# Kernel optimization log

Hardware: AMD Instinct MI355X
Metric: run time of the kernel (lower is better)

Reference implementation:

```python
import jax, jax.numpy as jnp
import numpy as np

NEG_SLOPE = 0.2
BN_EPS = 1e-5
SM_EPS = 1e-16


def gatv2_conv(x, src, dst, num_nodes, Wl, bl, Wr, br, att, bias, concat):
    # x: [N, Fin]; att: [H, C]
    H, C = att.shape
    xl = (x @ Wl + bl).reshape(-1, H, C)  # source-side (x_j), lin_l
    xr = (x @ Wr + br).reshape(-1, H, C)  # target-side (x_i), lin_r
    e = jax.nn.leaky_relu(xl[src] + xr[dst], NEG_SLOPE)          # [E, H, C]
    logits = jnp.einsum('ehc,hc->eh', e, att)                    # [E, H]
    m = jax.ops.segment_max(logits, dst, num_segments=num_nodes)  # [N, H]
    expv = jnp.exp(logits - m[dst])
    denom = jax.ops.segment_sum(expv, dst, num_segments=num_nodes)
    alpha = expv / (denom[dst] + SM_EPS)                          # [E, H]
    msg = xl[src] * alpha[:, :, None]                             # [E, H, C]
    out = jax.ops.segment_sum(msg, dst, num_segments=num_nodes)   # [N, H, C]
    out = out.reshape(num_nodes, H * C) if concat else out.mean(axis=1)
    return out + bias


def batchnorm(x, gamma, beta):
    mean = x.mean(axis=0)
    var = x.var(axis=0)  # biased, as torch uses for normalization
    return gamma * (x - mean) * jax.lax.rsqrt(var + BN_EPS) + beta


def setup_inputs() -> dict:
    key = jax.random.key(0)
    ks = jax.random.split(key, 16)
    N, E = 50000, 800000
    Fin, Hid, Out, H = 128, 64, 64, 4
    s = 0.05
    inp = {
        'x': jax.random.normal(ks[0], (N, Fin), jnp.float32),
        'edge_index': jax.random.randint(ks[1], (2, E), 0, N, jnp.int64),
        # conv1 (heads=4, concat=False)
        'Wl1': jax.random.normal(ks[2], (Fin, H * Hid), jnp.float32) * s,
        'bl1': jnp.zeros((H * Hid,), jnp.float32),
        'Wr1': jax.random.normal(ks[3], (Fin, H * Hid), jnp.float32) * s,
        'br1': jnp.zeros((H * Hid,), jnp.float32),
        'att1': jax.random.normal(ks[4], (H, Hid), jnp.float32) * s,
        'bias1': jnp.zeros((Hid,), jnp.float32),
        'g1': jnp.ones((Hid,), jnp.float32),
        'beta1': jnp.zeros((Hid,), jnp.float32),
        # conv2 (heads=1, concat=True -> same as single head)
        'Wl2': jax.random.normal(ks[5], (Hid, Out), jnp.float32) * s,
        'bl2': jnp.zeros((Out,), jnp.float32),
        'Wr2': jax.random.normal(ks[6], (Hid, Out), jnp.float32) * s,
        'br2': jnp.zeros((Out,), jnp.float32),
        'att2': jax.random.normal(ks[7], (1, Out), jnp.float32) * s,
        'bias2': jnp.zeros((Out,), jnp.float32),
        'g2': jnp.ones((Out,), jnp.float32),
        'beta2': jnp.zeros((Out,), jnp.float32),
    }
    return inp


def reference(x, edge_index, Wl1, bl1, Wr1, br1, att1, bias1, g1, beta1,
              Wl2, bl2, Wr2, br2, att2, bias2, g2, beta2):
    N = x.shape[0]
    loops = jnp.arange(N, dtype=edge_index.dtype)  # PyG add_self_loops=True
    src = jnp.concatenate([edge_index[0], loops])
    dst = jnp.concatenate([edge_index[1], loops])
    h = gatv2_conv(x, src, dst, N, Wl1, bl1, Wr1, br1, att1, bias1, concat=False)
    h = jax.nn.relu(batchnorm(h, g1, beta1))  # dropout = identity (eval)
    h = gatv2_conv(h, src, dst, N, Wl2, bl2, Wr2, br2, att2, bias2, concat=True)
    h = jax.nn.relu(batchnorm(h, g2, beta2))
    return h
```

## Files before the change

### kernel.cpp

```cpp
#include <hip/hip_runtime.h>
#include <hip/hip_bf16.h>
#include <math.h>

#define TPB 256

typedef __attribute__((ext_vector_type(8))) short bfrag8;
typedef __attribute__((ext_vector_type(4))) float f32x4;

static __device__ __forceinline__ float bf2f(unsigned int u) {
  union { unsigned int i; float f; } c; c.i = u << 16; return c.f;
}
static __device__ __forceinline__ unsigned short f2bf(float f) {
  union { float f; unsigned int i; } c; c.f = f;
  unsigned int lsb = (c.i >> 16) & 1u;
  return (unsigned short)((c.i + 0x7fffu + lsb) >> 16);
}
static __device__ __forceinline__ float lrelu(float v) {
  return v > 0.f ? v : 0.2f * v;
}

__global__ void k_deg(const int* __restrict__ ei, int E, int ET, int* __restrict__ deg) {
  int e = blockIdx.x * blockDim.x + threadIdx.x;
  if (e >= ET) return;
  int dst = (e < E) ? ei[E + e] : (e - E);
  atomicAdd(&deg[dst], 1);
}

__global__ void k_scan1(const int* __restrict__ deg, int N, int* __restrict__ bsum) {
  __shared__ int sm[TPB];
  int i = blockIdx.x * TPB + threadIdx.x;
  sm[threadIdx.x] = (i < N) ? deg[i] : 0;
  __syncthreads();
  for (int d = TPB / 2; d > 0; d >>= 1) {
    if (threadIdx.x < d) sm[threadIdx.x] += sm[threadIdx.x + d];
    __syncthreads();
  }
  if (threadIdx.x == 0) bsum[blockIdx.x] = sm[0];
}

__global__ void k_scan2(const int* __restrict__ bsum, int SB, int* __restrict__ bpre,
                        int* __restrict__ rowoff, int N) {
  __shared__ int sm[TPB];
  int v = (threadIdx.x < SB) ? bsum[threadIdx.x] : 0;
  sm[threadIdx.x] = v;
  __syncthreads();
  for (int d = 1; d < TPB; d <<= 1) {
    int t = (threadIdx.x >= d) ? sm[threadIdx.x - d] : 0;
    __syncthreads();
    sm[threadIdx.x] += t;
    __syncthreads();
  }
  if (threadIdx.x < SB) bpre[threadIdx.x] = sm[threadIdx.x] - v;
  if (threadIdx.x == SB - 1) rowoff[N] = sm[SB - 1];
}

__global__ void k_scan3(const int* __restrict__ deg, const int* __restrict__ bpre,
                        int N, int* __restrict__ rowoff, int* __restrict__ cursor) {
  __shared__ int sm[TPB];
  int i = blockIdx.x * TPB + threadIdx.x;
  int v = (i < N) ? deg[i] : 0;
  sm[threadIdx.x] = v;
  __syncthreads();
  for (int d = 1; d < TPB; d <<= 1) {
    int t = (threadIdx.x >= d) ? sm[threadIdx.x - d] : 0;
    __syncthreads();
    sm[threadIdx.x] += t;
    __syncthreads();
  }
  if (i < N) {
    int off = bpre[blockIdx.x] + sm[threadIdx.x] - v;
    rowoff[i] = off;
    cursor[i] = off;
  }
}

__global__ void k_fill(const int* __restrict__ ei, int E, int ET,
                       int* __restrict__ cursor, int* __restrict__ csrc) {
  int e = blockIdx.x * blockDim.x + threadIdx.x;
  if (e >= ET) return;
  int src, dst;
  if (e < E) { src = ei[e]; dst = ei[E + e]; } else { src = dst = e - E; }
  int pos = atomicAdd(&cursor[dst], 1);
  csrc[pos] = src;
}

__global__ void k_gemm_mfma(const float* __restrict__ A,
                            const float* __restrict__ W0, const float* __restrict__ b0,
                            const float* __restrict__ W1, const float* __restrict__ b1,
                            unsigned short* __restrict__ out0, unsigned short* __restrict__ out1,
                            int M, int K, int Nc, const float* __restrict__ affine) {
  __shared__ short As[64 * 128];
  __shared__ short Bls[64 * 128];
  __shared__ short Brs[64 * 128];
  const int r0 = blockIdx.x * 64, n0 = blockIdx.y * 64;
  const int tid = threadIdx.x;
  const int Kb = K * 2;

  const int kq = K >> 2;
  for (int idx = tid; idx < 16 * K; idx += TPB) {
    int row = idx / kq, c4 = idx - row * kq;
    int gr = r0 + row;
    float4 v = make_float4(0.f, 0.f, 0.f, 0.f);
    if (gr < M) v = *(const float4*)(A + (size_t)gr * K + c4 * 4);
    if (affine) {
      int c = c4 * 4;
      v.x = fmaxf(v.x * affine[c + 0] + affine[64 + c + 0], 0.f);
      v.y = fmaxf(v.y * affine[c + 1] + affine[64 + c + 1], 0.f);
      v.z = fmaxf(v.z * affine[c + 2] + affine[64 + c + 2], 0.f);
      v.w = fmaxf(v.w * affine[c + 3] + affine[64 + c + 3], 0.f);
    }
    ushort4 pk; pk.x = f2bf(v.x); pk.y = f2bf(v.y); pk.z = f2bf(v.z); pk.w = f2bf(v.w);
    int kb = (c4 * 8) ^ ((row & 7) << 4);
    *(ushort4*)((char*)As + row * Kb + kb) = pk;
  }
  for (int idx = tid; idx < 16 * K; idx += TPB) {
    int c = idx & 63, k4 = (idx >> 6) << 2;
    const float* p0 = W0 + (size_t)k4 * Nc + n0 + c;
    const float* p1 = W1 + (size_t)k4 * Nc + n0 + c;
    ushort4 pk0, pk1;
    pk0.x = f2bf(p0[0]); pk0.y = f2bf(p0[Nc]); pk0.z = f2bf(p0[2 * Nc]); pk0.w = f2bf(p0[3 * Nc]);
    pk1.x = f2bf(p1[0]); pk1.y = f2bf(p1[Nc]); pk1.z = f2bf(p1[2 * Nc]); pk1.w = f2bf(p1[3 * Nc]);
    int kb = (k4 * 2) ^ ((c & 7) << 4);
    *(ushort4*)((char*)Bls + c * Kb + kb) = pk0;
    *(ushort4*)((char*)Brs + c * Kb + kb) = pk1;
  }
  __syncthreads();

  const int w = tid >> 6, lane = tid & 63;
  const int arow = w * 16 + (lane & 15);
  const int l16 = (lane >> 4) << 3;
  f32x4 accL[4], accR[4];
#pragma unroll
  for (int i = 0; i < 4; ++i) { accL[i] = (f32x4)0.f; accR[i] = (f32x4)0.f; }
  for (int k0 = 0; k0 < K; k0 += 32) {
    int kb = (k0 + l16) * 2;
    bfrag8 af = *(bfrag8*)((char*)As + arow * Kb + (kb ^ ((arow & 7) << 4)));
#pragma unroll
    for (int cf = 0; cf < 4; ++cf) {
      int col = cf * 16 + (lane & 15);
      int cb = col * Kb + (kb ^ ((col & 7) << 4));
      bfrag8 bl = *(bfrag8*)((char*)Bls + cb);
      accL[cf] = __builtin_amdgcn_mfma_f32_16x16x32_bf16(af, bl, accL[cf], 0, 0, 0);
      bfrag8 br = *(bfrag8*)((char*)Brs + cb);
      accR[cf] = __builtin_amdgcn_mfma_f32_16x16x32_bf16(af, br, accR[cf], 0, 0, 0);
    }
  }
  const int rbase = r0 + w * 16 + ((lane >> 4) << 2);
  const int cbase = n0 + (lane & 15);
#pragma unroll
  for (int cf = 0; cf < 4; ++cf) {
    int gcol = cbase + cf * 16;
    float bb0 = b0[gcol], bb1 = b1[gcol];
#pragma unroll
    for (int r = 0; r < 4; ++r) {
      int grow = rbase + r;
      if (grow < M) {
        out0[(size_t)grow * Nc + gcol] = f2bf(accL[cf][r] + bb0);
        out1[(size_t)grow * Nc + gcol] = f2bf(accR[cf][r] + bb1);
      }
    }
  }
}

__global__ void k_gat1(const unsigned short* __restrict__ xl,
                       const unsigned short* __restrict__ xr,
                       const int* __restrict__ rowoff, const int* __restrict__ csrc,
                       const float* __restrict__ att, const float* __restrict__ bias,
                       float* __restrict__ out, int N) {
  int node = (blockIdx.x * blockDim.x + threadIdx.x) >> 6;
  int lane = threadIdx.x & 63;
  if (node >= N) return;
  int l4 = lane * 4;
  uint2 rv = *(const uint2*)(xr + (size_t)node * 256 + l4);
  float xr0 = bf2f(rv.x & 0xffffu), xr1 = bf2f(rv.x >> 16);
  float xr2 = bf2f(rv.y & 0xffffu), xr3 = bf2f(rv.y >> 16);
  float4 at = *(const float4*)(att + l4);
  int beg = rowoff[node], end = rowoff[node + 1];
  float s = 0.f, a0 = 0.f, a1 = 0.f, a2 = 0.f, a3 = 0.f;
  int k = beg;
  for (; k + 4 <= end; k += 4) {
    int srcs[4];
#pragma unroll
    for (int u = 0; u < 4; ++u) srcs[u] = csrc[k + u];
    uint2 vv[4];
#pragma unroll
    for (int u = 0; u < 4; ++u) vv[u] = *(const uint2*)(xl + (size_t)srcs[u] * 256 + l4);
    float xs[4][4], ps[4];
#pragma unroll
    for (int u = 0; u < 4; ++u) {
      xs[u][0] = bf2f(vv[u].x & 0xffffu); xs[u][1] = bf2f(vv[u].x >> 16);
      xs[u][2] = bf2f(vv[u].y & 0xffffu); xs[u][3] = bf2f(vv[u].y >> 16);
      ps[u] = lrelu(xs[u][0] + xr0) * at.x + lrelu(xs[u][1] + xr1) * at.y
            + lrelu(xs[u][2] + xr2) * at.z + lrelu(xs[u][3] + xr3) * at.w;
    }
#pragma unroll
    for (int u = 0; u < 4; ++u) {
      ps[u] += __shfl_xor(ps[u], 1); ps[u] += __shfl_xor(ps[u], 2);
      ps[u] += __shfl_xor(ps[u], 4); ps[u] += __shfl_xor(ps[u], 8);
    }
#pragma unroll
    for (int u = 0; u < 4; ++u) {
      float w = __expf(ps[u]);
      s += w;
      a0 += w * xs[u][0]; a1 += w * xs[u][1];
      a2 += w * xs[u][2]; a3 += w * xs[u][3];
    }
  }
  for (; k < end; ++k) {
    int src = csrc[k];
    uint2 v = *(const uint2*)(xl + (size_t)src * 256 + l4);
    float x0 = bf2f(v.x & 0xffffu), x1 = bf2f(v.x >> 16);
    float x2 = bf2f(v.y & 0xffffu), x3 = bf2f(v.y >> 16);
    float p = lrelu(x0 + xr0) * at.x + lrelu(x1 + xr1) * at.y
            + lrelu(x2 + xr2) * at.z + lrelu(x3 + xr3) * at.w;
    p += __shfl_xor(p, 1); p += __shfl_xor(p, 2);
    p += __shfl_xor(p, 4); p += __shfl_xor(p, 8);
    float w = __expf(p);
    s += w;
    a0 += w * x0; a1 += w * x1; a2 += w * x2; a3 += w * x3;
  }
  float inv = 1.f / (s + 1e-16f);
  a0 *= inv; a1 *= inv; a2 *= inv; a3 *= inv;
  a0 += __shfl_xor(a0, 16); a0 += __shfl_xor(a0, 32);
  a1 += __shfl_xor(a1, 16); a1 += __shfl_xor(a1, 32);
  a2 += __shfl_xor(a2, 16); a2 += __shfl_xor(a2, 32);
  a3 += __shfl_xor(a3, 16); a3 += __shfl_xor(a3, 32);
  if (lane < 16) {
    float4 o;
    o.x = a0 * 0.25f + bias[l4 + 0];
    o.y = a1 * 0.25f + bias[l4 + 1];
    o.z = a2 * 0.25f + bias[l4 + 2];
    o.w = a3 * 0.25f + bias[l4 + 3];
    *(float4*)(out + (size_t)node * 64 + l4) = o;
  }
}

__global__ void k_gat2(const unsigned short* __restrict__ xl,
                       const unsigned short* __restrict__ xr,
                       const int* __restrict__ rowoff, const int* __restrict__ csrc,
                       const float* __restrict__ att, const float* __restrict__ bias,
                       float* __restrict__ out, int N) {
  int node = (blockIdx.x * blockDim.x + threadIdx.x) >> 6;
  int lane = threadIdx.x & 63;
  if (node >= N) return;
  int grp = lane >> 4, c4 = (lane & 15) * 4;
  uint2 rv = *(const uint2*)(xr + (size_t)node * 64 + c4);
  float xr0 = bf2f(rv.x & 0xffffu), xr1 = bf2f(rv.x >> 16);
  float xr2 = bf2f(rv.y & 0xffffu), xr3 = bf2f(rv.y >> 16);
  float4 at = *(const float4*)(att + c4);
  int beg = rowoff[node], end = rowoff[node + 1];
  int iters = (end - beg + 3) >> 2;
  float s = 0.f, a0 = 0.f, a1 = 0.f, a2 = 0.f, a3 = 0.f;
  for (int it = 0; it < iters; ++it) {
    int kk = beg + it * 4 + grp;
    bool ok = kk < end;
    int src = ok ? csrc[kk] : 0;
    uint2 v = *(const uint2*)(xl + (size_t)src * 64 + c4);
    float x0 = bf2f(v.x & 0xffffu), x1 = bf2f(v.x >> 16);
    float x2 = bf2f(v.y & 0xffffu), x3 = bf2f(v.y >> 16);
    float p = lrelu(x0 + xr0) * at.x + lrelu(x1 + xr1) * at.y
            + lrelu(x2 + xr2) * at.z + lrelu(x3 + xr3) * at.w;
    p += __shfl_xor(p, 1); p += __shfl_xor(p, 2);
    p += __shfl_xor(p, 4); p += __shfl_xor(p, 8);
    float w = ok ? __expf(p) : 0.f;
    s += w;
    a0 += w * x0; a1 += w * x1; a2 += w * x2; a3 += w * x3;
  }
  s  += __shfl_xor(s, 16);  s  += __shfl_xor(s, 32);
  a0 += __shfl_xor(a0, 16); a0 += __shfl_xor(a0, 32);
  a1 += __shfl_xor(a1, 16); a1 += __shfl_xor(a1, 32);
  a2 += __shfl_xor(a2, 16); a2 += __shfl_xor(a2, 32);
  a3 += __shfl_xor(a3, 16); a3 += __shfl_xor(a3, 32);
  if (lane < 16) {
    float inv = 1.f / (s + 1e-16f);
    float4 o;
    o.x = a0 * inv + bias[c4 + 0];
    o.y = a1 * inv + bias[c4 + 1];
    o.z = a2 * inv + bias[c4 + 2];
    o.w = a3 * inv + bias[c4 + 3];
    *(float4*)(out + (size_t)node * 64 + c4) = o;
  }
}

__global__ void k_bnstat(const float* __restrict__ in, int N, float* __restrict__ part) {
  __shared__ float sm[TPB], sq[TPB];
  int col = threadIdx.x & 63;
  int rq = threadIdx.x >> 6;
  float s = 0.f, q = 0.f;
  for (int r = blockIdx.x * 4 + rq; r < N; r += gridDim.x * 4) {
    float v = in[(size_t)r * 64 + col];
    s += v; q += v * v;
  }
  sm[threadIdx.x] = s; sq[threadIdx.x] = q;
  __syncthreads();
  if (threadIdx.x < 64) {
    s = sm[threadIdx.x] + sm[threadIdx.x + 64] + sm[threadIdx.x + 128] + sm[threadIdx.x + 192];
    q = sq[threadIdx.x] + sq[threadIdx.x + 64] + sq[threadIdx.x + 128] + sq[threadIdx.x + 192];
    part[(size_t)blockIdx.x * 128 + threadIdx.x] = s;
    part[(size_t)blockIdx.x * 128 + 64 + threadIdx.x] = q;
  }
}

__global__ void k_bnfin(const float* __restrict__ part, int B, int N,
                        const float* __restrict__ g, const float* __restrict__ beta,
                        float* __restrict__ ab) {
  int c = threadIdx.x;
  float s = 0.f, q = 0.f;
  for (int b = 0; b < B; ++b) {
    s += part[(size_t)b * 128 + c];
    q += part[(size_t)b * 128 + 64 + c];
  }
  float mean = s / (float)N;
  float var = q / (float)N - mean * mean;
  float a = g[c] * rsqrtf(var + 1e-5f);
  ab[c] = a;
  ab[64 + c] = beta[c] - mean * a;
}

__global__ void k_bnapply(const float* __restrict__ in, const float* __restrict__ ab,
                          float* __restrict__ out, int total4) {
  int idx = blockIdx.x * blockDim.x + threadIdx.x;
  if (idx >= total4) return;
  float4 v = *(const float4*)(in + (size_t)idx * 4);
  int c0 = (idx & 15) * 4;
  v.x = fmaxf(v.x * ab[c0 + 0] + ab[64 + c0 + 0], 0.f);
  v.y = fmaxf(v.y * ab[c0 + 1] + ab[64 + c0 + 1], 0.f);
  v.z = fmaxf(v.z * ab[c0 + 2] + ab[64 + c0 + 2], 0.f);
  v.w = fmaxf(v.w * ab[c0 + 3] + ab[64 + c0 + 3], 0.f);
  *(float4*)(out + (size_t)idx * 4) = v;
}

extern "C" void kernel_launch(void* const* d_in, const int* in_sizes, int n_in,
                              void* d_out, int out_size, void* d_ws, size_t ws_size,
                              hipStream_t stream) {
  const float* x     = (const float*)d_in[0];
  const int*   ei    = (const int*)d_in[1];
  const float* Wl1   = (const float*)d_in[2];
  const float* bl1   = (const float*)d_in[3];
  const float* Wr1   = (const float*)d_in[4];
  const float* br1   = (const float*)d_in[5];
  const float* att1  = (const float*)d_in[6];
  const float* bias1 = (const float*)d_in[7];
  const float* g1    = (const float*)d_in[8];
  const float* be1   = (const float*)d_in[9];
  const float* Wl2   = (const float*)d_in[10];
  const float* bl2   = (const float*)d_in[11];
  const float* Wr2   = (const float*)d_in[12];
  const float* br2   = (const float*)d_in[13];
  const float* att2  = (const float*)d_in[14];
  const float* bias2 = (const float*)d_in[15];
  const float* g2    = (const float*)d_in[16];
  const float* be2   = (const float*)d_in[17];
  float* out = (float*)d_out;

  const int N  = in_sizes[0] / 128;
  const int E  = in_sizes[1] / 2;
  const int ET = E + N;
  const int SB = (N + TPB - 1) / TPB;

  char* p = (char*)d_ws;
  auto take = [&](size_t b) { char* q = p; p += (b + 255) & ~(size_t)255; return q; };

  unsigned short* xl1 = (unsigned short*)take((size_t)N * 256 * 2);
  unsigned short* xr1 = (unsigned short*)take((size_t)N * 256 * 2);
  unsigned short* xl2 = (unsigned short*)take((size_t)N * 64 * 2);
  unsigned short* xr2 = (unsigned short*)take((size_t)N * 64 * 2);
  float* out1 = (float*)take((size_t)N * 64 * 4);
  int* deg    = (int*)take((size_t)N * 4);
  int* rowoff = (int*)take((size_t)(N + 1) * 4);
  int* cursor = (int*)take((size_t)N * 4);
  int* csrc   = (int*)take((size_t)ET * 4);
  int* bsum   = (int*)take((size_t)SB * 4);
  int* bpre   = (int*)take((size_t)SB * 4);
  float* part = (float*)take((size_t)128 * 128 * 4);
  float* ab1  = (float*)take(128 * 4);
  float* ab2  = (float*)take(128 * 4);
  (void)ws_size; (void)n_in; (void)out_size;

  int egrid = (ET + TPB - 1) / TPB;
  int ngrid = (N + 3) / 4;
  int mtile = (N + 63) / 64;
  int total4 = N * 16;

  hipMemsetAsync(deg, 0, (size_t)N * 4, stream);
  k_deg<<<egrid, TPB, 0, stream>>>(ei, E, ET, deg);
  k_scan1<<<SB, TPB, 0, stream>>>(deg, N, bsum);
  k_scan2<<<1, TPB, 0, stream>>>(bsum, SB, bpre, rowoff, N);
  k_scan3<<<SB, TPB, 0, stream>>>(deg, bpre, N, rowoff, cursor);
  k_fill<<<egrid, TPB, 0, stream>>>(ei, E, ET, cursor, csrc);

  k_gemm_mfma<<<dim3(mtile, 4), TPB, 0, stream>>>(x, Wl1, bl1, Wr1, br1, xl1, xr1,
                                                  N, 128, 256, nullptr);
  k_gat1<<<ngrid, TPB, 0, stream>>>(xl1, xr1, rowoff, csrc, att1, bias1, out1, N);
  k_bnstat<<<128, TPB, 0, stream>>>(out1, N, part);
  k_bnfin<<<1, 64, 0, stream>>>(part, 128, N, g1, be1, ab1);

  k_gemm_mfma<<<dim3(mtile, 1), TPB, 0, stream>>>(out1, Wl2, bl2, Wr2, br2, xl2, xr2,
                                                  N, 64, 64, ab1);
  k_gat2<<<ngrid, TPB, 0, stream>>>(xl2, xr2, rowoff, csrc, att2, bias2, out, N);
  k_bnstat<<<128, TPB, 0, stream>>>(out, N, part);
  k_bnfin<<<1, 64, 0, stream>>>(part, 128, N, g2, be2, ab2);
  k_bnapply<<<(total4 + TPB - 1) / TPB, TPB, 0, stream>>>(out, ab2, out, total4);
}
```

Before: 406.9 us.

## Decompose leaky-ReLU attention, pre-convert operands to bf16, persistent GAT kernels

Rewrites leaky_relu(z) as 0.6z+0.4|z|. The linear part of the attention logit becomes per-node dot products (dl, dr), computed in the GEMM epilogue, so the per-edge work is one abs-weighted sum plus precomputed scalars. Inputs and transposed weights are converted to bf16 in a separate prep kernel, so the GEMM loads 16-byte chunks instead of converting fp32 strided data. The GAT kernels become grid-stride persistent loops with masked tails, and the scan merges scan2 into scan3 by having every block reduce its own prefix. The cost is extra prep passes and buffers, and a redundant prefix reduction in each block.

```diff
diff --git a/kernel.cpp b/kernel.cpp
--- a/kernel.cpp
+++ b/kernel.cpp
@@ -14,9 +14,6 @@
   union { float f; unsigned int i; } c; c.f = f;
   unsigned int lsb = (c.i >> 16) & 1u;
   return (unsigned short)((c.i + 0x7fffu + lsb) >> 16);
-}
-static __device__ __forceinline__ float lrelu(float v) {
-  return v > 0.f ? v : 0.2f * v;
 }
 
 __global__ void k_deg(const int* __restrict__ ei, int E, int ET, int* __restrict__ deg) {
@@ -38,40 +35,34 @@
   if (threadIdx.x == 0) bsum[blockIdx.x] = sm[0];
 }
 
-__global__ void k_scan2(const int* __restrict__ bsum, int SB, int* __restrict__ bpre,
-                        int* __restrict__ rowoff, int N) {
+__global__ void k_scan3(const int* __restrict__ deg, const int* __restrict__ bsum,
+                        int SB, int N, int* __restrict__ rowoff, int* __restrict__ cursor) {
   __shared__ int sm[TPB];
-  int v = (threadIdx.x < SB) ? bsum[threadIdx.x] : 0;
-  sm[threadIdx.x] = v;
+  int pv = (threadIdx.x < blockIdx.x) ? bsum[threadIdx.x] : 0;
+  sm[threadIdx.x] = pv;
   __syncthreads();
-  for (int d = 1; d < TPB; d <<= 1) {
-    int t = (threadIdx.x >= d) ? sm[threadIdx.x - d] : 0;
+  for (int dd = TPB / 2; dd > 0; dd >>= 1) {
+    if (threadIdx.x < dd) sm[threadIdx.x] += sm[threadIdx.x + dd];
     __syncthreads();
-    sm[threadIdx.x] += t;
-    __syncthreads();
-  }
-  if (threadIdx.x < SB) bpre[threadIdx.x] = sm[threadIdx.x] - v;
-  if (threadIdx.x == SB - 1) rowoff[N] = sm[SB - 1];
-}
-
-__global__ void k_scan3(const int* __restrict__ deg, const int* __restrict__ bpre,
-                        int N, int* __restrict__ rowoff, int* __restrict__ cursor) {
-  __shared__ int sm[TPB];
+  }
+  int base = sm[0];
+  __syncthreads();
   int i = blockIdx.x * TPB + threadIdx.x;
   int v = (i < N) ? deg[i] : 0;
   sm[threadIdx.x] = v;
   __syncthreads();
-  for (int d = 1; d < TPB; d <<= 1) {
-    int t = (threadIdx.x >= d) ? sm[threadIdx.x - d] : 0;
+  for (int dd = 1; dd < TPB; dd <<= 1) {
+    int t = (threadIdx.x >= dd) ? sm[threadIdx.x - dd] : 0;
     __syncthreads();
     sm[threadIdx.x] += t;
     __syncthreads();
   }
   if (i < N) {
-    int off = bpre[blockIdx.x] + sm[threadIdx.x] - v;
+    int off = base + sm[threadIdx.x] - v;
     rowoff[i] = off;
     cursor[i] = off;
   }
+  if (blockIdx.x == SB - 1 && threadIdx.x == TPB - 1) rowoff[N] = base + sm[TPB - 1];
 }
 
 __global__ void k_fill(const int* __restrict__ ei, int E, int ET,
@@ -84,45 +75,78 @@
   csrc[pos] = src;
 }
 
-__global__ void k_gemm_mfma(const float* __restrict__ A,
-                            const float* __restrict__ W0, const float* __restrict__ b0,
-                            const float* __restrict__ W1, const float* __restrict__ b1,
+__global__ void k_prep1(const float* __restrict__ x,
+                        const float* __restrict__ Wl1, const float* __restrict__ Wr1,
+                        const float* __restrict__ Wl2, const float* __restrict__ Wr2,
+                        unsigned short* __restrict__ xb,
+                        unsigned short* __restrict__ wt1l, unsigned short* __restrict__ wt1r,
+                        unsigned short* __restrict__ wt2l, unsigned short* __restrict__ wt2r,
+                        int nx4) {
+  int i = blockIdx.x * blockDim.x + threadIdx.x;
+  int stride = gridDim.x * blockDim.x;
+  int wtot = nx4 + 65536 + 8192;
+  for (; i < wtot; i += stride) {
+    if (i < nx4) {
+      float4 v = *(const float4*)(x + (size_t)i * 4);
+      ushort4 o; o.x = f2bf(v.x); o.y = f2bf(v.y); o.z = f2bf(v.z); o.w = f2bf(v.w);
+      *(ushort4*)(xb + (size_t)i * 4) = o;
+    } else if (i < nx4 + 32768) {
+      int j = i - nx4; int c = j >> 7, k = j & 127;
+      wt1l[j] = f2bf(Wl1[(size_t)k * 256 + c]);
+    } else if (i < nx4 + 65536) {
+      int j = i - nx4 - 32768; int c = j >> 7, k = j & 127;
+      wt1r[j] = f2bf(Wr1[(size_t)k * 256 + c]);
+    } else if (i < nx4 + 65536 + 4096) {
+      int j = i - nx4 - 65536; int c = j >> 6, k = j & 63;
+      wt2l[j] = f2bf(Wl2[(size_t)k * 64 + c]);
+    } else {
+      int j = i - nx4 - 69632; int c = j >> 6, k = j & 63;
+      wt2r[j] = f2bf(Wr2[(size_t)k * 64 + c]);
+    }
+  }
+}
+
+__global__ void k_prep2(const float* __restrict__ in, const float* __restrict__ ab,
+                        unsigned short* __restrict__ o, int n4) {
+  int i = blockIdx.x * blockDim.x + threadIdx.x;
+  if (i >= n4) return;
+  float4 v = *(const float4*)(in + (size_t)i * 4);
+  int c0 = (i & 15) * 4;
+  ushort4 u;
+  u.x = f2bf(fmaxf(v.x * ab[c0 + 0] + ab[64 + c0 + 0], 0.f));
+  u.y = f2bf(fmaxf(v.y * ab[c0 + 1] + ab[64 + c0 + 1], 0.f));
+  u.z = f2bf(fmaxf(v.z * ab[c0 + 2] + ab[64 + c0 + 2], 0.f));
+  u.w = f2bf(fmaxf(v.w * ab[c0 + 3] + ab[64 + c0 + 3], 0.f));
+  *(ushort4*)(o + (size_t)i * 4) = u;
+}
+
+__global__ void k_gemm_mfma(const unsigned short* __restrict__ Ab,
+                            const unsigned short* __restrict__ Wt0, const float* __restrict__ b0,
+                            const unsigned short* __restrict__ Wt1, const float* __restrict__ b1,
+                            const float* __restrict__ att,
+                            float* __restrict__ dl, float* __restrict__ dr,
                             unsigned short* __restrict__ out0, unsigned short* __restrict__ out1,
-                            int M, int K, int Nc, const float* __restrict__ affine) {
-  __shared__ short As[64 * 128];
-  __shared__ short Bls[64 * 128];
-  __shared__ short Brs[64 * 128];
+                            int M, int K, int Nc, int Hs) {
+  extern __shared__ short lds[];
+  short* As = lds;
+  short* Bls = lds + 64 * K;
+  short* Brs = lds + 128 * K;
   const int r0 = blockIdx.x * 64, n0 = blockIdx.y * 64;
   const int tid = threadIdx.x;
   const int Kb = K * 2;
-
-  const int kq = K >> 2;
-  for (int idx = tid; idx < 16 * K; idx += TPB) {
-    int row = idx / kq, c4 = idx - row * kq;
+  const int cpr = K >> 3;
+  const int chunks = 64 * cpr;
+  for (int idx = tid; idx < chunks; idx += TPB) {
+    int row = idx / cpr, k8 = (idx - row * cpr) * 8;
+    int kb = (k8 * 2) ^ ((row & 7) << 4);
     int gr = r0 + row;
-    float4 v = make_float4(0.f, 0.f, 0.f, 0.f);
-    if (gr < M) v = *(const float4*)(A + (size_t)gr * K + c4 * 4);
-    if (affine) {
-      int c = c4 * 4;
-      v.x = fmaxf(v.x * affine[c + 0] + affine[64 + c + 0], 0.f);
-      v.y = fmaxf(v.y * affine[c + 1] + affine[64 + c + 1], 0.f);
-      v.z = fmaxf(v.z * affine[c + 2] + affine[64 + c + 2], 0.f);
-      v.w = fmaxf(v.w * affine[c + 3] + affine[64 + c + 3], 0.f);
-    }
-    ushort4 pk; pk.x = f2bf(v.x); pk.y = f2bf(v.y); pk.z = f2bf(v.z); pk.w = f2bf(v.w);
-    int kb = (c4 * 8) ^ ((row & 7) << 4);
-    *(ushort4*)((char*)As + row * Kb + kb) = pk;
-  }
-  for (int idx = tid; idx < 16 * K; idx += TPB) {
-    int c = idx & 63, k4 = (idx >> 6) << 2;
-    const float* p0 = W0 + (size_t)k4 * Nc + n0 + c;
-    const float* p1 = W1 + (size_t)k4 * Nc + n0 + c;
-    ushort4 pk0, pk1;
-    pk0.x = f2bf(p0[0]); pk0.y = f2bf(p0[Nc]); pk0.z = f2bf(p0[2 * Nc]); pk0.w = f2bf(p0[3 * Nc]);
-    pk1.x = f2bf(p1[0]); pk1.y = f2bf(p1[Nc]); pk1.z = f2bf(p1[2 * Nc]); pk1.w = f2bf(p1[3 * Nc]);
-    int kb = (k4 * 2) ^ ((c & 7) << 4);
-    *(ushort4*)((char*)Bls + c * Kb + kb) = pk0;
-    *(ushort4*)((char*)Brs + c * Kb + kb) = pk1;
+    uint4 av = make_uint4(0, 0, 0, 0);
+    if (gr < M) av = *(const uint4*)(Ab + (size_t)gr * K + k8);
+    *(uint4*)((char*)As + row * Kb + kb) = av;
+    uint4 w0 = *(const uint4*)(Wt0 + (size_t)(n0 + row) * K + k8);
+    *(uint4*)((char*)Bls + row * Kb + kb) = w0;
+    uint4 w1 = *(const uint4*)(Wt1 + (size_t)(n0 + row) * K + k8);
+    *(uint4*)((char*)Brs + row * Kb + kb) = w1;
   }
   __syncthreads();
 
@@ -147,16 +171,39 @@
   }
   const int rbase = r0 + w * 16 + ((lane >> 4) << 2);
   const int cbase = n0 + (lane & 15);
+  float tL[4] = {0.f, 0.f, 0.f, 0.f}, tR[4] = {0.f, 0.f, 0.f, 0.f};
 #pragma unroll
   for (int cf = 0; cf < 4; ++cf) {
     int gcol = cbase + cf * 16;
-    float bb0 = b0[gcol], bb1 = b1[gcol];
+    float bb0 = b0[gcol], bb1 = b1[gcol], aa = att[gcol];
+#pragma unroll
+    for (int r = 0; r < 4; ++r) {
+      float oL = accL[cf][r] + bb0, oR = accR[cf][r] + bb1;
+      int grow = rbase + r;
+      if (grow < M) {
+        out0[(size_t)grow * Nc + gcol] = f2bf(oL);
+        out1[(size_t)grow * Nc + gcol] = f2bf(oR);
+      }
+      tL[r] += oL * aa;
+      tR[r] += oR * aa;
+    }
+  }
+#pragma unroll
+  for (int r = 0; r < 4; ++r) {
+#pragma unroll
+    for (int d = 1; d < 16; d <<= 1) {
+      tL[r] += __shfl_xor(tL[r], d);
+      tR[r] += __shfl_xor(tR[r], d);
+    }
+  }
+  if ((lane & 15) == 0) {
+    int h = n0 >> 6;
 #pragma unroll
     for (int r = 0; r < 4; ++r) {
       int grow = rbase + r;
       if (grow < M) {
-        out0[(size_t)grow * Nc + gcol] = f2bf(accL[cf][r] + bb0);
-        out1[(size_t)grow * Nc + gcol] = f2bf(accR[cf][r] + bb1);
+        dl[(size_t)grow * Hs + h] = 0.6f * tL[r];
+        dr[(size_t)grow * Hs + h] = 0.6f * tR[r];
       }
     }
   }
@@ -164,121 +211,165 @@
 
 __global__ void k_gat1(const unsigned short* __restrict__ xl,
                        const unsigned short* __restrict__ xr,
+                       const float* __restrict__ dl, const float* __restrict__ dr,
                        const int* __restrict__ rowoff, const int* __restrict__ csrc,
                        const float* __restrict__ att, const float* __restrict__ bias,
-                       float* __restrict__ out, int N) {
-  int node = (blockIdx.x * blockDim.x + threadIdx.x) >> 6;
+                       float* __restrict__ out, int N, int nw) {
+  int wid = (blockIdx.x * blockDim.x + threadIdx.x) >> 6;
   int lane = threadIdx.x & 63;
-  if (node >= N) return;
-  int l4 = lane * 4;
-  uint2 rv = *(const uint2*)(xr + (size_t)node * 256 + l4);
-  float xr0 = bf2f(rv.x & 0xffffu), xr1 = bf2f(rv.x >> 16);
-  float xr2 = bf2f(rv.y & 0xffffu), xr3 = bf2f(rv.y >> 16);
-  float4 at = *(const float4*)(att + l4);
-  int beg = rowoff[node], end = rowoff[node + 1];
-  float s = 0.f, a0 = 0.f, a1 = 0.f, a2 = 0.f, a3 = 0.f;
-  int k = beg;
-  for (; k + 4 <= end; k += 4) {
-    int srcs[4];
-#pragma unroll
-    for (int u = 0; u < 4; ++u) srcs[u] = csrc[k + u];
-    uint2 vv[4];
-#pragma unroll
-    for (int u = 0; u < 4; ++u) vv[u] = *(const uint2*)(xl + (size_t)srcs[u] * 256 + l4);
-    float xs[4][4], ps[4];
-#pragma unroll
-    for (int u = 0; u < 4; ++u) {
-      xs[u][0] = bf2f(vv[u].x & 0xffffu); xs[u][1] = bf2f(vv[u].x >> 16);
-      xs[u][2] = bf2f(vv[u].y & 0xffffu); xs[u][3] = bf2f(vv[u].y >> 16);
-      ps[u] = lrelu(xs[u][0] + xr0) * at.x + lrelu(xs[u][1] + xr1) * at.y
-            + lrelu(xs[u][2] + xr2) * at.z + lrelu(xs[u][3] + xr3) * at.w;
-    }
-#pragma unroll
-    for (int u = 0; u < 4; ++u) {
-      ps[u] += __shfl_xor(ps[u], 1); ps[u] += __shfl_xor(ps[u], 2);
-      ps[u] += __shfl_xor(ps[u], 4); ps[u] += __shfl_xor(ps[u], 8);
-    }
-#pragma unroll
-    for (int u = 0; u < 4; ++u) {
-      float w = __expf(ps[u]);
-      s += w;
-      a0 += w * xs[u][0]; a1 += w * xs[u][1];
-      a2 += w * xs[u][2]; a3 += w * xs[u][3];
-    }
-  }
-  for (; k < end; ++k) {
-    int src = csrc[k];
-    uint2 v = *(const uint2*)(xl + (size_t)src * 256 + l4);
-    float x0 = bf2f(v.x & 0xffffu), x1 = bf2f(v.x >> 16);
-    float x2 = bf2f(v.y & 0xffffu), x3 = bf2f(v.y >> 16);
-    float p = lrelu(x0 + xr0) * at.x + lrelu(x1 + xr1) * at.y
-            + lrelu(x2 + xr2) * at.z + lrelu(x3 + xr3) * at.w;
-    p += __shfl_xor(p, 1); p += __shfl_xor(p, 2);
-    p += __shfl_xor(p, 4); p += __shfl_xor(p, 8);
-    float w = __expf(p);
-    s += w;
-    a0 += w * x0; a1 += w * x1; a2 += w * x2; a3 += w * x3;
-  }
-  float inv = 1.f / (s + 1e-16f);
-  a0 *= inv; a1 *= inv; a2 *= inv; a3 *= inv;
-  a0 += __shfl_xor(a0, 16); a0 += __shfl_xor(a0, 32);
-  a1 += __shfl_xor(a1, 16); a1 += __shfl_xor(a1, 32);
-  a2 += __shfl_xor(a2, 16); a2 += __shfl_xor(a2, 32);
-  a3 += __shfl_xor(a3, 16); a3 += __shfl_xor(a3, 32);
-  if (lane < 16) {
-    float4 o;
-    o.x = a0 * 0.25f + bias[l4 + 0];
-    o.y = a1 * 0.25f + bias[l4 + 1];
-    o.z = a2 * 0.25f + bias[l4 + 2];
-    o.w = a3 * 0.25f + bias[l4 + 3];
-    *(float4*)(out + (size_t)node * 64 + l4) = o;
+  int l4 = lane * 4, hid = lane >> 4;
+  float4 atv = *(const float4*)(att + l4);
+  float atx = 0.4f * atv.x, aty = 0.4f * atv.y, atz = 0.4f * atv.z, atw = 0.4f * atv.w;
+  float4 bb = *(const float4*)(bias + l4);
+  for (int node = wid; node < N; node += nw) {
+    uint2 rv = *(const uint2*)(xr + (size_t)node * 256 + l4);
+    float xr0 = bf2f(rv.x & 0xffffu), xr1 = bf2f(rv.x >> 16);
+    float xr2 = bf2f(rv.y & 0xffffu), xr3 = bf2f(rv.y >> 16);
+    float drv = dr[node * 4 + hid];
+    int beg = rowoff[node], end = rowoff[node + 1];
+    float s = 0.f, a0 = 0.f, a1 = 0.f, a2 = 0.f, a3 = 0.f;
+    int k = beg;
+    for (; k + 4 <= end; k += 4) {
+      int srcs[4]; uint2 vv[4]; float dls[4], ps[4];
+#pragma unroll
+      for (int u = 0; u < 4; ++u) srcs[u] = csrc[k + u];
+#pragma unroll
+      for (int u = 0; u < 4; ++u) {
+        vv[u] = *(const uint2*)(xl + (size_t)srcs[u] * 256 + l4);
+        dls[u] = dl[srcs[u] * 4 + hid];
+      }
+#pragma unroll
+      for (int u = 0; u < 4; ++u) {
+        float x0 = bf2f(vv[u].x & 0xffffu), x1 = bf2f(vv[u].x >> 16);
+        float x2 = bf2f(vv[u].y & 0xffffu), x3 = bf2f(vv[u].y >> 16);
+        ps[u] = atx * fabsf(x0 + xr0) + aty * fabsf(x1 + xr1)
+              + atz * fabsf(x2 + xr2) + atw * fabsf(x3 + xr3);
+      }
+#pragma unroll
+      for (int u = 0; u < 4; ++u) {
+        ps[u] += __shfl_xor(ps[u], 1); ps[u] += __shfl_xor(ps[u], 2);
+        ps[u] += __shfl_xor(ps[u], 4); ps[u] += __shfl_xor(ps[u], 8);
+      }
+#pragma unroll
+      for (int u = 0; u < 4; ++u) {
+        float wv = __expf(ps[u] + dls[u] + drv);
+        float x0 = bf2f(vv[u].x & 0xffffu), x1 = bf2f(vv[u].x >> 16);
+        float x2 = bf2f(vv[u].y & 0xffffu), x3 = bf2f(vv[u].y >> 16);
+        s += wv; a0 += wv * x0; a1 += wv * x1; a2 += wv * x2; a3 += wv * x3;
+      }
+    }
+    if (k < end) {
+      int srcs[4]; uint2 vv[4]; float dls[4], ps[4]; bool okv[4];
+#pragma unroll
+      for (int u = 0; u < 4; ++u) {
+        okv[u] = (k + u) < end;
+        srcs[u] = okv[u] ? csrc[k + u] : 0;
+      }
+#pragma unroll
+      for (int u = 0; u < 4; ++u) {
+        vv[u] = *(const uint2*)(xl + (size_t)srcs[u] * 256 + l4);
+        dls[u] = dl[srcs[u] * 4 + hid];
+      }
+#pragma unroll
+      for (int u = 0; u < 4; ++u) {
+        float x0 = bf2f(vv[u].x & 0xffffu), x1 = bf2f(vv[u].x >> 16);
+        float x2 = bf2f(vv[u].y & 0xffffu), x3 = bf2f(vv[u].y >> 16);
+        ps[u] = atx * fabsf(x0 + xr0) + aty * fabsf(x1 + xr1)
+              + atz * fabsf(x2 + xr2) + atw * fabsf(x3 + xr3);
+      }
+#pragma unroll
+      for (int u = 0; u < 4; ++u) {
+        ps[u] += __shfl_xor(ps[u], 1); ps[u] += __shfl_xor(ps[u], 2);
+        ps[u] += __shfl_xor(ps[u], 4); ps[u] += __shfl_xor(ps[u], 8);
+      }
+#pragma unroll
+      for (int u = 0; u < 4; ++u) {
+        float wv = okv[u] ? __expf(ps[u] + dls[u] + drv) : 0.f;
+        float x0 = bf2f(vv[u].x & 0xffffu), x1 = bf2f(vv[u].x >> 16);
+        float x2 = bf2f(vv[u].y & 0xffffu), x3 = bf2f(vv[u].y >> 16);
+        s += wv; a0 += wv * x0; a1 += wv * x1; a2 += wv * x2; a3 += wv * x3;
+      }
+    }
+    float inv = 1.f / (s + 1e-16f);
+    a0 *= inv; a1 *= inv; a2 *= inv; a3 *= inv;
+    a0 += __shfl_xor(a0, 16); a0 += __shfl_xor(a0, 32);
+    a1 += __shfl_xor(a1, 16); a1 += __shfl_xor(a1, 32);
+    a2 += __shfl_xor(a2, 16); a2 += __shfl_xor(a2, 32);
+    a3 += __shfl_xor(a3, 16); a3 += __shfl_xor(a3, 32);
+    if (lane < 16) {
+      float4 o;
+      o.x = a0 * 0.25f + bb.x;
+      o.y = a1 * 0.25f + bb.y;
+      o.z = a2 * 0.25f + bb.z;
+      o.w = a3 * 0.25f + bb.w;
+      *(float4*)(out + (size_t)node * 64 + l4) = o;
+    }
   }
 }
 
 __global__ void k_gat2(const unsigned short* __restrict__ xl,
                        const unsigned short* __restrict__ xr,
+                       const float* __restrict__ dl, const float* __restrict__ dr,
                        const int* __restrict__ rowoff, const int* __restrict__ csrc,
                        const float* __restrict__ att, const float* __restrict__ bias,
-                       float* __restrict__ out, int N) {
-  int node = (blockIdx.x * blockDim.x + threadIdx.x) >> 6;
+                       float* __restrict__ out, int N, int nw) {
+  int wid = (blockIdx.x * blockDim.x + threadIdx.x) >> 6;
   int lane = threadIdx.x & 63;
-  if (node >= N) return;
   int grp = lane >> 4, c4 = (lane & 15) * 4;
-  uint2 rv = *(const uint2*)(xr + (size_t)node * 64 + c4);
-  float xr0 = bf2f(rv.x & 0xffffu), xr1 = bf2f(rv.x >> 16);
-  float xr2 = bf2f(rv.y & 0xffffu), xr3 = bf2f(rv.y >> 16);
-  float4 at = *(const float4*)(att + c4);
-  int beg = rowoff[node], end = rowoff[node + 1];
-  int iters = (end - beg + 3) >> 2;
-  float s = 0.f, a0 = 0.f, a1 = 0.f, a2 = 0.f, a3 = 0.f;
-  for (int it = 0; it < iters; ++it) {
-    int kk = beg + it * 4 + grp;
-    bool ok = kk < end;
-    int src = ok ? csrc[kk] : 0;
-    uint2 v = *(const uint2*)(xl + (size_t)src * 64 + c4);
-    float x0 = bf2f(v.x & 0xffffu), x1 = bf2f(v.x >> 16);
-    float x2 = bf2f(v.y & 0xffffu), x3 = bf2f(v.y >> 16);
-    float p = lrelu(x0 + xr0) * at.x + lrelu(x1 + xr1) * at.y
-            + lrelu(x2 + xr2) * at.z + lrelu(x3 + xr3) * at.w;
-    p += __shfl_xor(p, 1); p += __shfl_xor(p, 2);
-    p += __shfl_xor(p, 4); p += __shfl_xor(p, 8);
-    float w = ok ? __expf(p) : 0.f;
-    s += w;
-    a0 += w * x0; a1 += w * x1; a2 += w * x2; a3 += w * x3;
-  }
-  s  += __shfl_xor(s, 16);  s  += __shfl_xor(s, 32);
-  a0 += __shfl_xor(a0, 16); a0 += __shfl_xor(a0, 32);
-  a1 += __shfl_xor(a1, 16); a1 += __shfl_xor(a1, 32);
-  a2 += __shfl_xor(a2, 16); a2 += __shfl_xor(a2, 32);
-  a3 += __shfl_xor(a3, 16); a3 += __shfl_xor(a3, 32);
-  if (lane < 16) {
-    float inv = 1.f / (s + 1e-16f);
-    float4 o;
-    o.x = a0 * inv + bias[c4 + 0];
-    o.y = a1 * inv + bias[c4 + 1];
-    o.z = a2 * inv + bias[c4 + 2];
-    o.w = a3 * inv + bias[c4 + 3];
-    *(float4*)(out + (size_t)node * 64 + c4) = o;
+  float4 atv = *(const float4*)(att + c4);
+  float atx = 0.4f * atv.x, aty = 0.4f * atv.y, atz = 0.4f * atv.z, atw = 0.4f * atv.w;
+  float4 bb = *(const float4*)(bias + c4);
+  for (int node = wid; node < N; node += nw) {
+    uint2 rv = *(const uint2*)(xr + (size_t)node * 64 + c4);
+    float xr0 = bf2f(rv.x & 0xffffu), xr1 = bf2f(rv.x >> 16);
+    float xr2 = bf2f(rv.y & 0xffffu), xr3 = bf2f(rv.y >> 16);
+    float drv = dr[node];
+    int beg = rowoff[node], end = rowoff[node + 1];
+    int nf = (end - beg) >> 2;
+    float s = 0.f, a0 = 0.f, a1 = 0.f, a2 = 0.f, a3 = 0.f;
+    for (int it = 0; it < nf; ++it) {
+      int kk = beg + it * 4 + grp;
+      int src = csrc[kk];
+      float dlv = dl[src];
+      uint2 v = *(const uint2*)(xl + (size_t)src * 64 + c4);
+      float x0 = bf2f(v.x & 0xffffu), x1 = bf2f(v.x >> 16);
+      float x2 = bf2f(v.y & 0xffffu), x3 = bf2f(v.y >> 16);
+      float p = atx * fabsf(x0 + xr0) + aty * fabsf(x1 + xr1)
+              + atz * fabsf(x2 + xr2) + atw * fabsf(x3 + xr3);
+      p += __shfl_xor(p, 1); p += __shfl_xor(p, 2);
+      p += __shfl_xor(p, 4); p += __shfl_xor(p, 8);
+      float wv = __expf(p + dlv + drv);
+      s += wv; a0 += wv * x0; a1 += wv * x1; a2 += wv * x2; a3 += wv * x3;
+    }
+    if ((end - beg) & 3) {
+      int kk = beg + nf * 4 + grp;
+      bool ok = kk < end;
+      int src = ok ? csrc[kk] : 0;
+      float dlv = dl[src];
+      uint2 v = *(const uint2*)(xl + (size_t)src * 64 + c4);
+      float x0 = bf2f(v.x & 0xffffu), x1 = bf2f(v.x >> 16);
+      float x2 = bf2f(v.y & 0xffffu), x3 = bf2f(v.y >> 16);
+      float p = atx * fabsf(x0 + xr0) + aty * fabsf(x1 + xr1)
+              + atz * fabsf(x2 + xr2) + atw * fabsf(x3 + xr3);
+      p += __shfl_xor(p, 1); p += __shfl_xor(p, 2);
+      p += __shfl_xor(p, 4); p += __shfl_xor(p, 8);
+      float wv = ok ? __expf(p + dlv + drv) : 0.f;
+      s += wv; a0 += wv * x0; a1 += wv * x1; a2 += wv * x2; a3 += wv * x3;
+    }
+    s  += __shfl_xor(s, 16);  s  += __shfl_xor(s, 32);
+    a0 += __shfl_xor(a0, 16); a0 += __shfl_xor(a0, 32);
+    a1 += __shfl_xor(a1, 16); a1 += __shfl_xor(a1, 32);
+    a2 += __shfl_xor(a2, 16); a2 += __shfl_xor(a2, 32);
+    a3 += __shfl_xor(a3, 16); a3 += __shfl_xor(a3, 32);
+    if (lane < 16) {
+      float inv = 1.f / (s + 1e-16f);
+      float4 o;
+      o.x = a0 * inv + bb.x;
+      o.y = a1 * inv + bb.y;
+      o.z = a2 * inv + bb.z;
+      o.w = a3 * inv + bb.w;
+      *(float4*)(out + (size_t)node * 64 + c4) = o;
+    }
   }
 }
 
@@ -366,38 +457,53 @@
   unsigned short* xl2 = (unsigned short*)take((size_t)N * 64 * 2);
   unsigned short* xr2 = (unsigned short*)take((size_t)N * 64 * 2);
   float* out1 = (float*)take((size_t)N * 64 * 4);
+  unsigned short* xb = (unsigned short*)take((size_t)N * 128 * 2);
+  unsigned short* wt1l = (unsigned short*)take(256 * 128 * 2);
+  unsigned short* wt1r = (unsigned short*)take(256 * 128 * 2);
+  unsigned short* wt2l = (unsigned short*)take(64 * 64 * 2);
+  unsigned short* wt2r = (unsigned short*)take(64 * 64 * 2);
+  float* dl1 = (float*)take((size_t)N * 4 * 4);
+  float* dr1 = (float*)take((size_t)N * 4 * 4);
+  float* dl2 = (float*)take((size_t)N * 4);
+  float* dr2 = (float*)take((size_t)N * 4);
   int* deg    = (int*)take((size_t)N * 4);
   int* rowoff = (int*)take((size_t)(N + 1) * 4);
   int* cursor = (int*)take((size_t)N * 4);
   int* csrc   = (int*)take((size_t)ET * 4);
   int* bsum   = (int*)take((size_t)SB * 4);
-  int* bpre   = (int*)take((size_t)SB * 4);
   float* part = (float*)take((size_t)128 * 128 * 4);
   float* ab1  = (float*)take(128 * 4);
   float* ab2  = (float*)take(128 * 4);
   (void)ws_size; (void)n_in; (void)out_size;
 
+  unsigned short* A2 = xb;
+
   int egrid = (ET + TPB - 1) / TPB;
-  int ngrid = (N + 3) / 4;
   int mtile = (N + 63) / 64;
   int total4 = N * 16;
+  int nx4 = N * 32;
+  int wtot = nx4 + 65536 + 8192;
+  const int GATB = 2048, NW = GATB * (TPB / 64);
 
   hipMemsetAsync(deg, 0, (size_t)N * 4, stream);
   k_deg<<<egrid, TPB, 0, stream>>>(ei, E, ET, deg);
   k_scan1<<<SB, TPB, 0, stream>>>(deg, N, bsum);
-  k_scan2<<<1, TPB, 0, stream>>>(bsum, SB, bpre, rowoff, N);
-  k_scan3<<<SB, TPB, 0, stream>>>(deg, bpre, N, rowoff, cursor);
+  k_scan3<<<SB, TPB, 0, stream>>>(deg, bsum, SB, N, rowoff, cursor);
   k_fill<<<egrid, TPB, 0, stream>>>(ei, E, ET, cursor, csrc);
 
-  k_gemm_mfma<<<dim3(mtile, 4), TPB, 0, stream>>>(x, Wl1, bl1, Wr1, br1, xl1, xr1,
-                                                  N, 128, 256, nullptr);
-  k_gat1<<<ngrid, TPB, 0, stream>>>(xl1, xr1, rowoff, csrc, att1, bias1, out1, N);
+  k_prep1<<<(wtot + TPB - 1) / TPB, TPB, 0, stream>>>(x, Wl1, Wr1, Wl2, Wr2,
+                                                      xb, wt1l, wt1r, wt2l, wt2r, nx4);
+
+  k_gemm_mfma<<<dim3(mtile, 4), TPB, 3 * 64 * 128 * 2, stream>>>(
+      xb, wt1l, bl1, wt1r, br1, att1, dl1, dr1, xl1, xr1, N, 128, 256, 4);
+  k_gat1<<<GATB, TPB, 0, stream>>>(xl1, xr1, dl1, dr1, rowoff, csrc, att1, bias1, out1, N, NW);
   k_bnstat<<<128, TPB, 0, stream>>>(out1, N, part);
   k_bnfin<<<1, 64, 0, stream>>>(part, 128, N, g1, be1, ab1);
 
-  k_gemm_mfma<<<dim3(mtile, 1), TPB, 0, stream>>>(out1, Wl2, bl2, Wr2, br2, xl2, xr2,
-                                                  N, 64, 64, ab1);
-  k_gat2<<<ngrid, TPB, 0, stream>>>(xl2, xr2, rowoff, csrc, att2, bias2, out, N);
+  k_prep2<<<(total4 + TPB - 1) / TPB, TPB, 0, stream>>>(out1, ab1, A2, total4);
+  k_gemm_mfma<<<dim3(mtile, 1), TPB, 3 * 64 * 64 * 2, stream>>>(
+      A2, wt2l, bl2, wt2r, br2, att2, dl2, dr2, xl2, xr2, N, 64, 64, 1);
+  k_gat2<<<GATB, TPB, 0, stream>>>(xl2, xr2, dl2, dr2, rowoff, csrc, att2, bias2, out, N, NW);
   k_bnstat<<<128, TPB, 0, stream>>>(out, N, part);
   k_bnfin<<<1, 64, 0, stream>>>(part, 128, N, g2, be2, ab2);
   k_bnapply<<<(total4 + TPB - 1) / TPB, TPB, 0, stream>>>(out, ab2, out, total4);
```

New measurement: 405.1 us. No clear change (-0.4%).
